# Kernel optimization log

Measured on AMD Instinct MI355X. Metric: run time of the kernel, lower is better.

The kernel has to match this reference:

```python
import jax, jax.numpy as jnp
import numpy as np
import math

EMBED = 256
NH = 8      # num_heads
NP = 4      # num_points
HD = EMBED // NH  # head_dim = 32
BS = 8
NQ = 8192
HH = 128
WW = 128


def setup_inputs() -> dict:
    key = jax.random.key(0)
    ks = jax.random.split(key, 12)
    query = jax.random.normal(ks[0], (BS, NQ, EMBED), jnp.float32)
    reference_points = jax.random.uniform(ks[1], (BS, NQ, 2), dtype=jnp.float32)
    value = jax.random.normal(ks[2], (BS, HH * WW, EMBED), jnp.float32)
    # sampling_offsets: torch init uses zero weight + structured bias (rose pattern);
    # use small random weight so the math path is exercised, keep the structured bias.
    w_off = 0.001 * jax.random.normal(ks[3], (EMBED, NH * NP * 2), jnp.float32)
    thetas = np.arange(NH, dtype=np.float32) * (2.0 * math.pi / NH)
    grid = np.stack([np.cos(thetas), np.sin(thetas)], -1)          # [NH, 2]
    grid = np.tile(grid[:, None, :], (1, NP, 1)) * np.arange(1, NP + 1, dtype=np.float32)[None, :, None]
    b_off = jnp.asarray(grid.reshape(-1), jnp.float32)              # [NH*NP*2]
    w_attn = 0.01 * jax.random.normal(ks[4], (EMBED, NH * NP), jnp.float32)
    b_attn = jnp.zeros((NH * NP,), jnp.float32)
    xav = 1.0 / math.sqrt(EMBED)
    w_val = xav * jax.random.normal(ks[5], (EMBED, EMBED), jnp.float32)
    b_val = jnp.zeros((EMBED,), jnp.float32)
    w_out = xav * jax.random.normal(ks[6], (EMBED, EMBED), jnp.float32)
    b_out = jnp.zeros((EMBED,), jnp.float32)
    return {"query": query, "reference_points": reference_points, "value": value,
            "w_off": w_off, "b_off": b_off, "w_attn": w_attn, "b_attn": b_attn,
            "w_val": w_val, "b_val": b_val, "w_out": w_out, "b_out": b_out,
            "H": HH, "W": WW}


def _deform_attn(query, reference_points, value, w_off, b_off, w_attn, b_attn,
                 w_val, b_val, w_out, b_out, H, W):
    bs, nq, _ = query.shape
    # value projection -> [bs, nh, H*W, hd]
    v = (value @ w_val + b_val).reshape(bs, H * W, NH, HD).transpose(0, 2, 1, 3)
    # offsets and attention weights
    off = (query @ w_off + b_off).reshape(bs, nq, NH, NP, 2)
    attn = jax.nn.softmax((query @ w_attn + b_attn).reshape(bs, nq, NH, NP), axis=-1)
    norm = jnp.array([W, H], dtype=query.dtype)
    loc = reference_points[:, :, None, None, :] + off / norm       # [bs,nq,nh,np,2] in [0,1]
    # grid_sample, align_corners=False: pixel = loc*size - 0.5  (x <-> W, y <-> H)
    px = (loc[..., 0] * W - 0.5).transpose(0, 2, 1, 3).reshape(bs, NH, nq * NP)
    py = (loc[..., 1] * H - 0.5).transpose(0, 2, 1, 3).reshape(bs, NH, nq * NP)
    x0 = jnp.floor(px); y0 = jnp.floor(py)
    wx = px - x0; wy = py - y0
    x0i = x0.astype(jnp.int32); y0i = y0.astype(jnp.int32)

    def gather(xi, yi):
        # padding_mode='zeros': out-of-range corners contribute 0
        mask = ((xi >= 0) & (xi < W) & (yi >= 0) & (yi < H)).astype(v.dtype)
        idx = jnp.clip(yi, 0, H - 1) * W + jnp.clip(xi, 0, W - 1)   # [bs,nh,K]
        g = jnp.take_along_axis(v, idx[..., None], axis=2)          # [bs,nh,K,hd]
        return g * mask[..., None]

    samp = (((1 - wx) * (1 - wy))[..., None] * gather(x0i, y0i)
            + (wx * (1 - wy))[..., None] * gather(x0i + 1, y0i)
            + ((1 - wx) * wy)[..., None] * gather(x0i, y0i + 1)
            + (wx * wy)[..., None] * gather(x0i + 1, y0i + 1))      # [bs,nh,nq*np,hd]
    samp = samp.reshape(bs, NH, nq, NP, HD)
    aw = attn.transpose(0, 2, 1, 3)                                 # [bs,nh,nq,np]
    out = jnp.einsum('bhqpd,bhqp->bqhd', samp, aw).reshape(bs, nq, EMBED)
    return out @ w_out + b_out


def reference(query, reference_points, value, w_off, b_off, w_attn, b_attn,
              w_val, b_val, w_out, b_out, H, W):
    return _deform_attn(query, reference_points, value, w_off, b_off, w_attn, b_attn,
                        w_val, b_val, w_out, b_out, H, W)
```

## Files before the change

### kernel.cpp

```cpp
#include <hip/hip_runtime.h>
#include <stdint.h>

#define NQ 8192
#define BSZ 8
#define NH 8
#define NP 4
#define HD 32
#define EMBED 256
#define IMG 128
#define NPIX (IMG*IMG)

typedef __attribute__((ext_vector_type(8))) short short8v;
typedef __attribute__((ext_vector_type(4))) float f32x4;

static __device__ __forceinline__ float bf2f(uint32_t u) {
    union { uint32_t i; float f; } x; x.i = u << 16; return x.f;
}
static __device__ __forceinline__ uint16_t f2bf(float f) {
    union { float f; uint32_t i; } x; x.f = f;
    uint32_t r = x.i + 0x7fffu + ((x.i >> 16) & 1u);
    return (uint16_t)(r >> 16);
}
static __device__ __forceinline__ uint32_t cvtpk(float lo, float hi) {
    uint32_t r;
    asm("v_cvt_pk_bf16_f32 %0, %1, %2" : "=v"(r) : "v"(lo), "v"(hi));
    return r;
}
static __device__ __forceinline__ void gload_lds16(const void* g, void* l) {
    __builtin_amdgcn_global_load_lds(
        (const __attribute__((address_space(1))) unsigned int*)g,
        (__attribute__((address_space(3))) unsigned int*)l, 16, 0, 0);
}

#define WAITV(n) asm volatile("s_waitcnt vmcnt(" #n ")" ::: "memory")
#define WAITLGKM() do { asm volatile("s_waitcnt lgkmcnt(0)" ::: "memory"); \
                        __builtin_amdgcn_sched_barrier(0); } while (0)
#define BARRIER() do { __builtin_amdgcn_s_barrier(); \
                       __builtin_amdgcn_sched_barrier(0); } while (0)

static __device__ __forceinline__ void waitv_n(int n) {
    switch (n) {
        case 0: WAITV(0); break;  case 1: WAITV(1); break;
        case 2: WAITV(2); break;  case 3: WAITV(3); break;
        case 4: WAITV(4); break;  default: WAITV(5); break;
    }
}

__global__ void pack_w(const float* __restrict__ w_val, const float* __restrict__ w_out,
                       const float* __restrict__ w_off, const float* __restrict__ w_attn,
                       uint16_t* __restrict__ wTval, uint16_t* __restrict__ wTout,
                       uint16_t* __restrict__ wTcat) {
    int k = blockIdx.x;
    int n = threadIdx.x;
    wTval[n * 256 + k] = f2bf(w_val[k * 256 + n]);
    wTout[n * 256 + k] = f2bf(w_out[k * 256 + n]);
    if (n < 64)       wTcat[n * 256 + k]        = f2bf(w_off[k * 64 + n]);
    else if (n < 96)  wTcat[n * 256 + k]        = f2bf(w_attn[k * 32 + (n - 64)]);
}

__global__ __launch_bounds__(256)
void cvt_kernel(const float* __restrict__ in, uint16_t* __restrict__ out, int n8) {
    int i = blockIdx.x * 256 + threadIdx.x;
    const int stride = gridDim.x * 256;
    for (; i < n8; i += stride) {
        const float4* p = (const float4*)in + (size_t)i * 2;
        float4 a = p[0], b = p[1];
        uint4 o;
        o.x = cvtpk(a.x, a.y); o.y = cvtpk(a.z, a.w);
        o.z = cvtpk(b.x, b.y); o.w = cvtpk(b.z, b.w);
        ((uint4*)out)[i] = o;
    }
}

template<bool OUT_F32, bool PLANE, int STRIPES>
__global__ __launch_bounds__(512, 2)
void gemm_bf16(const uint16_t* __restrict__ Ap, const uint16_t* __restrict__ BT,
               void* __restrict__ Cp, const float* __restrict__ bias) {
    constexpr int T = STRIPES * 4;
    __shared__ char SMEM[131072 + (PLANE ? 32768 : 0)];
    char* ring = SMEM;
    const int tid = threadIdx.x, w = tid >> 6, l = tid & 63;
    const int stripe0 = blockIdx.x * STRIPES;

    auto grow0 = [&](int t) { return (stripe0 + (t >> 2)) * 64 + (t & 3) * 16; };
    auto stageA = [&](int t) {
        const char* src = (const char*)Ap + (size_t)(grow0(t) + (l & 15)) * 512
                          + w * 64 + (l >> 4) * 16;
        gload_lds16(src, ring + (t & 15) * 8192 + w * 1024);
    };

#pragma unroll
    for (int c = 0; c < 16; ++c) {
        int loff = c * 8192 + tid * 16;
        int row = loff >> 9, x = loff & 511;
        const char* src = (const char*)BT + (size_t)row * 512 + (x ^ ((row & 7) << 4));
        gload_lds16(src, SMEM + c * 8192 + w * 1024);
    }
    WAITV(0);
    BARRIER();
    short8v breg[2][8];
#pragma unroll
    for (int n = 0; n < 2; ++n) {
        int col = w * 32 + n * 16 + (l & 15);
        const char* base = SMEM + col * 512;
        const int sz = (col & 7) << 4;
#pragma unroll
        for (int k = 0; k < 8; ++k)
            breg[n][k] = *(const short8v*)(base + ((k * 64 + (l >> 4) * 16) ^ sz));
    }
    WAITLGKM();
    BARRIER();
#pragma unroll
    for (int t = 0; t < 6; ++t) stageA(t);

    for (int st = 0; st < STRIPES; ++st) {
        f32x4 acc[4][2] = {};
#pragma unroll
        for (int s = 0; s < 4; ++s) {
            const int t = st * 4 + s;
            const int rem = T - 1 - t;
            waitv_n(rem < 5 ? rem : 5);
            BARRIER();
            if (t + 6 < T) stageA(t + 6);
            const char* abase = ring + (t & 15) * 8192 + l * 16;
            short8v a[8];
#pragma unroll
            for (int k = 0; k < 8; ++k)
                a[k] = *(const short8v*)(abase + k * 1024);
#pragma unroll
            for (int k = 0; k < 8; ++k)
#pragma unroll
                for (int n = 0; n < 2; ++n)
                    acc[s][n] = __builtin_amdgcn_mfma_f32_16x16x32_bf16(a[k], breg[n][k], acc[s][n], 0, 0, 0);
        }

        const int gr0 = (stripe0 + st) * 64;
        if constexpr (PLANE) {
            char* Cs = SMEM + 131072;
#pragma unroll
            for (int s = 0; s < 4; ++s)
#pragma unroll
                for (int n = 0; n < 2; ++n) {
                    int lcol = w * 32 + n * 16 + (l & 15);
                    float bv = bias[lcol];
#pragma unroll
                    for (int r = 0; r < 4; ++r) {
                        int lrow = s * 16 + (l >> 4) * 4 + r;
                        *(uint16_t*)(Cs + ((lrow * 512 + lcol * 2) ^ ((lrow & 7) << 4)))
                            = f2bf(acc[s][n][r] + bv);
                    }
                }
            WAITLGKM();
            BARRIER();
            const int b_ = gr0 >> 14, pix0 = gr0 & 16383;
            char* pb = (char*)Cp + (((size_t)(b_ * 8 + w)) << 20) + (size_t)pix0 * 64;
#pragma unroll
            for (int i = 0; i < 4; ++i) {
                int fb = i * 1024 + l * 16;
                int lrow = fb >> 6, x = w * 64 + (fb & 63);
                uint4 d = *(const uint4*)(Cs + ((lrow * 512 + x) ^ ((lrow & 7) << 4)));
                *(uint4*)(pb + (size_t)lrow * 64 + (fb & 63)) = d;
            }
            WAITLGKM();
            BARRIER();
        } else {
#pragma unroll
            for (int s = 0; s < 4; ++s)
#pragma unroll
                for (int n = 0; n < 2; ++n) {
                    int col = w * 32 + n * 16 + (l & 15);
                    float bv = bias[col];
#pragma unroll
                    for (int r = 0; r < 4; ++r) {
                        int gr = gr0 + s * 16 + (l >> 4) * 4 + r;
                        float val = acc[s][n][r] + bv;
                        if constexpr (OUT_F32)
                            ((float*)Cp)[(size_t)gr * 256 + col] = val;
                        else
                            ((uint16_t*)Cp)[(size_t)gr * 256 + col] = f2bf(val);
                    }
                }
        }
    }
}

__global__ __launch_bounds__(256, 2)
void proj_kernel(const float* __restrict__ Q, const uint16_t* __restrict__ WTcat,
                 const float* __restrict__ b_off, const float* __restrict__ b_attn,
                 const float* __restrict__ refp,
                 float* __restrict__ locs, float* __restrict__ attnw) {
    __shared__ uint16_t Bs[96 * 256];
    __shared__ uint16_t As[64 * 256];
    const int tid = threadIdx.x, w = tid >> 6, l = tid & 63;
    const int blk = blockIdx.x;

#pragma unroll
    for (int c = 0; c < 12; ++c) {
        int loff = (w * 12 + c) * 1024;
        int lofl = loff + l * 16;
        int row = lofl >> 9, colb = lofl & 511;
        const char* src = (const char*)WTcat + (size_t)row * 512 + (colb ^ ((row & 7) << 4));
        gload_lds16(src, (char*)Bs + loff);
    }
#pragma unroll
    for (int c = 0; c < 8; ++c) {
        int loff = tid * 16 + c * 4096;
        int row = loff >> 9, colb = loff & 511;
        const float* src = Q + (size_t)(blk * 64 + row) * 256 + (colb >> 1);
        float4 f0 = *(const float4*)src;
        float4 f1 = *(const float4*)(src + 4);
        uint4 pk;
        pk.x = (uint32_t)f2bf(f0.x) | ((uint32_t)f2bf(f0.y) << 16);
        pk.y = (uint32_t)f2bf(f0.z) | ((uint32_t)f2bf(f0.w) << 16);
        pk.z = (uint32_t)f2bf(f1.x) | ((uint32_t)f2bf(f1.y) << 16);
        pk.w = (uint32_t)f2bf(f1.z) | ((uint32_t)f2bf(f1.w) << 16);
        *(uint4*)((char*)As + row * 512 + (colb ^ ((row & 7) << 4))) = pk;
    }
    __syncthreads();

    f32x4 acc[6] = {};
    const int arow = w * 16 + (l & 15);
#pragma unroll
    for (int ks = 0; ks < 8; ++ks) {
        const int kb = ks * 64 + (l >> 4) * 16;
        short8v a = *(const short8v*)((const char*)As + arow * 512 + (kb ^ ((arow & 7) << 4)));
#pragma unroll
        for (int n = 0; n < 6; ++n) {
            int col = n * 16 + (l & 15);
            short8v b = *(const short8v*)((const char*)Bs + col * 512 + (kb ^ ((col & 7) << 4)));
            acc[n] = __builtin_amdgcn_mfma_f32_16x16x32_bf16(a, b, acc[n], 0, 0, 0);
        }
    }
    __syncthreads();
    float* scores = (float*)As;
#pragma unroll
    for (int n = 0; n < 6; ++n)
#pragma unroll
        for (int r = 0; r < 4; ++r)
            scores[(w * 16 + (l >> 4) * 4 + r) * 96 + n * 16 + (l & 15)] = acc[n][r];
    __syncthreads();

    for (int it = tid; it < 512; it += 256) {
        int row = it >> 3, h = it & 7;
        int gq = blk * 64 + row;
        int b = gq >> 13, q = gq & 8191;
        size_t itemH = ((size_t)(b * 8 + h) << 13) | q;
        float s0 = scores[row * 96 + 64 + h * 4 + 0] + b_attn[h * 4 + 0];
        float s1 = scores[row * 96 + 64 + h * 4 + 1] + b_attn[h * 4 + 1];
        float s2 = scores[row * 96 + 64 + h * 4 + 2] + b_attn[h * 4 + 2];
        float s3 = scores[row * 96 + 64 + h * 4 + 3] + b_attn[h * 4 + 3];
        float mx = fmaxf(fmaxf(s0, s1), fmaxf(s2, s3));
        float e0 = __expf(s0 - mx), e1 = __expf(s1 - mx);
        float e2 = __expf(s2 - mx), e3 = __expf(s3 - mx);
        float inv = 1.0f / (e0 + e1 + e2 + e3);
        float rx = refp[gq * 2 + 0] * 128.0f - 0.5f;
        float ry = refp[gq * 2 + 1] * 128.0f - 0.5f;
        float ew[4] = { e0, e1, e2, e3 };
#pragma unroll
        for (int p = 0; p < 4; ++p) {
            float ox = scores[row * 96 + h * 8 + p * 2 + 0] + b_off[h * 8 + p * 2 + 0];
            float oy = scores[row * 96 + h * 8 + p * 2 + 1] + b_off[h * 8 + p * 2 + 1];
            locs[itemH * 8 + p * 2 + 0] = rx + ox;
            locs[itemH * 8 + p * 2 + 1] = ry + oy;
            attnw[itemH * 4 + p] = ew[p] * inv;
        }
    }
}

__global__ __launch_bounds__(256)
void sample_kernel(const uint16_t* __restrict__ v, const float* __restrict__ locs,
                   const float* __restrict__ attnw, uint16_t* __restrict__ oatt) {
    const int bid = blockIdx.x;
    const int h = bid & 7;
    const int rest = bid >> 3;
    const int b = rest >> 7;
    const int chunk = rest & 127;
    const int qloc = threadIdx.x >> 2;
    const int dg = threadIdx.x & 3;
    const int q = chunk * 64 + qloc;
    const size_t itemH = ((size_t)(b * 8 + h) << 13) | q;
    const char* plane = (const char*)v + ((size_t)(b * 8 + h) << 20);

    float4 l01 = ((const float4*)locs)[itemH * 2 + 0];
    float4 l23 = ((const float4*)locs)[itemH * 2 + 1];
    float4 aw4 = ((const float4*)attnw)[itemH];
    float pxs[4] = { l01.x, l01.z, l23.x, l23.z };
    float pys[4] = { l01.y, l01.w, l23.y, l23.w };
    float aws[4] = { aw4.x, aw4.y, aw4.z, aw4.w };

    float acc[8] = {};
#pragma unroll
    for (int p = 0; p < 4; ++p) {
        float px = pxs[p], py = pys[p], aw = aws[p];
        float fx = floorf(px), fy = floorf(py);
        float wx = px - fx, wy = py - fy;
        int x0 = (int)fx, y0 = (int)fy;
#pragma unroll
        for (int cy = 0; cy < 2; ++cy) {
            int yy = y0 + cy;
            float wyv = cy ? wy : 1.f - wy;
            bool yok = (unsigned)yy < (unsigned)IMG;
            int yc = min(max(yy, 0), IMG - 1);
#pragma unroll
            for (int cx = 0; cx < 2; ++cx) {
                int xx = x0 + cx;
                bool ok = yok && ((unsigned)xx < (unsigned)IMG);
                int xc = min(max(xx, 0), IMG - 1);
                float wgt = ok ? aw * (cx ? wx : 1.f - wx) * wyv : 0.f;
                const uint4 u = *(const uint4*)(plane + ((size_t)(yc * IMG + xc) << 6) + dg * 16);
                acc[0] += wgt * bf2f(u.x & 0xffffu);
                acc[1] += wgt * bf2f(u.x >> 16);
                acc[2] += wgt * bf2f(u.y & 0xffffu);
                acc[3] += wgt * bf2f(u.y >> 16);
                acc[4] += wgt * bf2f(u.z & 0xffffu);
                acc[5] += wgt * bf2f(u.z >> 16);
                acc[6] += wgt * bf2f(u.w & 0xffffu);
                acc[7] += wgt * bf2f(u.w >> 16);
            }
        }
    }
    const size_t bq = (size_t)b * NQ + q;
    uint4 out;
    out.x = (uint32_t)f2bf(acc[0]) | ((uint32_t)f2bf(acc[1]) << 16);
    out.y = (uint32_t)f2bf(acc[2]) | ((uint32_t)f2bf(acc[3]) << 16);
    out.z = (uint32_t)f2bf(acc[4]) | ((uint32_t)f2bf(acc[5]) << 16);
    out.w = (uint32_t)f2bf(acc[6]) | ((uint32_t)f2bf(acc[7]) << 16);
    *(uint4*)((char*)oatt + (bq * 256 + h * 32 + dg * 8) * 2) = out;
}

extern "C" void kernel_launch(void* const* d_in, const int* in_sizes, int n_in,
                              void* d_out, int out_size, void* d_ws, size_t ws_size,
                              hipStream_t stream) {
    const float* query  = (const float*)d_in[0];
    const float* refp   = (const float*)d_in[1];
    const float* value  = (const float*)d_in[2];
    const float* w_off  = (const float*)d_in[3];
    const float* b_off  = (const float*)d_in[4];
    const float* w_attn = (const float*)d_in[5];
    const float* b_attn = (const float*)d_in[6];
    const float* w_val  = (const float*)d_in[7];
    const float* b_val  = (const float*)d_in[8];
    const float* w_out  = (const float*)d_in[9];
    const float* b_out  = (const float*)d_in[10];

    char* ws = (char*)d_ws;
    uint16_t* v     = (uint16_t*)(ws);
    uint16_t* oatt  = (uint16_t*)(ws + (64u << 20));
    float*    locs  = (float*)(ws + (96u << 20));
    float*    attnw = (float*)(ws + (112u << 20));
    uint16_t* wTval = (uint16_t*)(ws + (120u << 20));
    uint16_t* wTout = (uint16_t*)(ws + (120u << 20) + 131072);
    uint16_t* wTcat = (uint16_t*)(ws + (120u << 20) + 262144);
    uint16_t* abf16 = (uint16_t*)(ws + (192u << 20));

    pack_w<<<256, 256, 0, stream>>>(w_val, w_out, w_off, w_attn, wTval, wTout, wTcat);
    cvt_kernel<<<4096, 256, 0, stream>>>(value, abf16, 131072 * 256 / 8);
    gemm_bf16<false, true, 8><<<256, 512, 0, stream>>>(abf16, wTval, v, b_val);
    proj_kernel<<<1024, 256, 0, stream>>>(query, wTcat, b_off, b_attn, refp, locs, attnw);
    sample_kernel<<<8192, 256, 0, stream>>>(v, locs, attnw, oatt);
    gemm_bf16<true, false, 4><<<256, 512, 0, stream>>>(oatt, wTout, (float*)d_out, b_out);
}
```

Before: 165.0 us.

## Deepen GEMM A-prefetch pipeline and stage epilogue stores through LDS

The bf16 GEMM template gains slot-count and prefetch-depth parameters, so the value projection keeps 14 tiles in flight and the output projection 10, up from 6, and the stripe loop is unrolled. The fp32 output epilogue now writes results into swizzled LDS and then issues coalesced 16-byte row stores instead of scattered scalar stores. The plane epilogue is remapped so each thread writes across head planes. Launch bounds drop to one block per CU because LDS usage grows, which trades occupancy for deeper in-flight memory traffic.

```diff
diff --git a/kernel.cpp b/kernel.cpp
--- a/kernel.cpp
+++ b/kernel.cpp
@@ -40,9 +40,13 @@
 
 static __device__ __forceinline__ void waitv_n(int n) {
     switch (n) {
-        case 0: WAITV(0); break;  case 1: WAITV(1); break;
-        case 2: WAITV(2); break;  case 3: WAITV(3); break;
-        case 4: WAITV(4); break;  default: WAITV(5); break;
+        case 0:  WAITV(0);  break;  case 1:  WAITV(1);  break;
+        case 2:  WAITV(2);  break;  case 3:  WAITV(3);  break;
+        case 4:  WAITV(4);  break;  case 5:  WAITV(5);  break;
+        case 6:  WAITV(6);  break;  case 7:  WAITV(7);  break;
+        case 8:  WAITV(8);  break;  case 9:  WAITV(9);  break;
+        case 10: WAITV(10); break;  case 11: WAITV(11); break;
+        case 12: WAITV(12); break;  default: WAITV(13); break;
     }
 }
 
@@ -72,12 +76,13 @@
     }
 }
 
-template<bool OUT_F32, bool PLANE, int STRIPES>
-__global__ __launch_bounds__(512, 2)
+template<bool OUT_F32, bool PLANE, int STRIPES, int SLOTS, int DEPTH>
+__global__ __launch_bounds__(512, 1)
 void gemm_bf16(const uint16_t* __restrict__ Ap, const uint16_t* __restrict__ BT,
                void* __restrict__ Cp, const float* __restrict__ bias) {
     constexpr int T = STRIPES * 4;
-    __shared__ char SMEM[131072 + (PLANE ? 32768 : 0)];
+    constexpr int CB = PLANE ? 32768 : 65536;
+    __shared__ char SMEM[SLOTS * 8192 + CB];
     char* ring = SMEM;
     const int tid = threadIdx.x, w = tid >> 6, l = tid & 63;
     const int stripe0 = blockIdx.x * STRIPES;
@@ -86,7 +91,7 @@
     auto stageA = [&](int t) {
         const char* src = (const char*)Ap + (size_t)(grow0(t) + (l & 15)) * 512
                           + w * 64 + (l >> 4) * 16;
-        gload_lds16(src, ring + (t & 15) * 8192 + w * 1024);
+        gload_lds16(src, ring + (t % SLOTS) * 8192 + w * 1024);
     };
 
 #pragma unroll
@@ -111,18 +116,19 @@
     WAITLGKM();
     BARRIER();
 #pragma unroll
-    for (int t = 0; t < 6; ++t) stageA(t);
-
+    for (int t = 0; t < DEPTH; ++t) stageA(t);
+
+#pragma unroll
     for (int st = 0; st < STRIPES; ++st) {
         f32x4 acc[4][2] = {};
 #pragma unroll
         for (int s = 0; s < 4; ++s) {
             const int t = st * 4 + s;
             const int rem = T - 1 - t;
-            waitv_n(rem < 5 ? rem : 5);
-            BARRIER();
-            if (t + 6 < T) stageA(t + 6);
-            const char* abase = ring + (t & 15) * 8192 + l * 16;
+            waitv_n(rem < DEPTH - 1 ? rem : DEPTH - 1);
+            BARRIER();
+            if (t + DEPTH < T) stageA(t + DEPTH);
+            const char* abase = ring + (t % SLOTS) * 8192 + l * 16;
             short8v a[8];
 #pragma unroll
             for (int k = 0; k < 8; ++k)
@@ -136,7 +142,7 @@
 
         const int gr0 = (stripe0 + st) * 64;
         if constexpr (PLANE) {
-            char* Cs = SMEM + 131072;
+            char* Cs = SMEM + SLOTS * 8192;
 #pragma unroll
             for (int s = 0; s < 4; ++s)
 #pragma unroll
@@ -156,30 +162,44 @@
             char* pb = (char*)Cp + (((size_t)(b_ * 8 + w)) << 20) + (size_t)pix0 * 64;
 #pragma unroll
             for (int i = 0; i < 4; ++i) {
-                int fb = i * 1024 + l * 16;
-                int lrow = fb >> 6, x = w * 64 + (fb & 63);
+                int fb = i * 8192 + tid * 16;
+                int lrow = fb >> 6, x = fb & 63;
+                lrow = fb >> 9; x = fb & 511;
                 uint4 d = *(const uint4*)(Cs + ((lrow * 512 + x) ^ ((lrow & 7) << 4)));
-                *(uint4*)(pb + (size_t)lrow * 64 + (fb & 63)) = d;
+                int h_off = x >> 6, dbyte = x & 63;
+                char* dst = (char*)Cp + (((size_t)(b_ * 8 + h_off)) << 20)
+                            + (size_t)(pix0 + lrow) * 64 + dbyte;
+                *(uint4*)dst = d;
             }
             WAITLGKM();
             BARRIER();
         } else {
+            char* Cs = SMEM + SLOTS * 8192;
 #pragma unroll
             for (int s = 0; s < 4; ++s)
 #pragma unroll
                 for (int n = 0; n < 2; ++n) {
-                    int col = w * 32 + n * 16 + (l & 15);
-                    float bv = bias[col];
+                    int lcol = w * 32 + n * 16 + (l & 15);
+                    float bv = bias[lcol];
 #pragma unroll
                     for (int r = 0; r < 4; ++r) {
-                        int gr = gr0 + s * 16 + (l >> 4) * 4 + r;
-                        float val = acc[s][n][r] + bv;
-                        if constexpr (OUT_F32)
-                            ((float*)Cp)[(size_t)gr * 256 + col] = val;
-                        else
-                            ((uint16_t*)Cp)[(size_t)gr * 256 + col] = f2bf(val);
+                        int lrow = s * 16 + (l >> 4) * 4 + r;
+                        *(float*)(Cs + ((lrow * 1024 + lcol * 4) ^ ((lrow & 7) << 4)))
+                            = acc[s][n][r] + bv;
                     }
                 }
+            WAITLGKM();
+            BARRIER();
+            float* Cg = (float*)Cp + (size_t)gr0 * 256;
+#pragma unroll
+            for (int i = 0; i < 8; ++i) {
+                int fb = i * 8192 + tid * 16;
+                int lrow = fb >> 10, x = fb & 1023;
+                uint4 d = *(const uint4*)(Cs + ((lrow * 1024 + x) ^ ((lrow & 7) << 4)));
+                *(uint4*)((char*)(Cg + (size_t)lrow * 256) + x) = d;
+            }
+            WAITLGKM();
+            BARRIER();
         }
     }
 }
@@ -355,8 +375,8 @@
 
     pack_w<<<256, 256, 0, stream>>>(w_val, w_out, w_off, w_attn, wTval, wTout, wTcat);
     cvt_kernel<<<4096, 256, 0, stream>>>(value, abf16, 131072 * 256 / 8);
-    gemm_bf16<false, true, 8><<<256, 512, 0, stream>>>(abf16, wTval, v, b_val);
+    gemm_bf16<false, true, 8, 16, 14><<<256, 512, 0, stream>>>(abf16, wTval, v, b_val);
     proj_kernel<<<1024, 256, 0, stream>>>(query, wTcat, b_off, b_attn, refp, locs, attnw);
     sample_kernel<<<8192, 256, 0, stream>>>(v, locs, attnw, oatt);
-    gemm_bf16<true, false, 4><<<256, 512, 0, stream>>>(oatt, wTout, (float*)d_out, b_out);
-}
+    gemm_bf16<true, false, 4, 12, 10><<<256, 512, 0, stream>>>(oatt, wTout, (float*)d_out, b_out);
+}
```

Result: no change. 165.1 us (+0.0%).
